# Kernel optimization log

Measured on AMD Instinct MI355X. Metric: run time of the kernel, lower is better.

## Reference

```python
import jax, jax.numpy as jnp
import numpy as np

N_NODES = 100000
IN_DIM = 500
HID_DIM = 128
OUT_DIM = 40
N_EDGES = 1600000


def setup_inputs() -> dict:
    key = jax.random.key(0)
    k1, k2, k3, k4, k5 = jax.random.split(key, 5)
    x = jax.random.normal(k1, (N_NODES, IN_DIM), dtype=jnp.float32)
    edge_index = jax.random.randint(k2, (2, N_EDGES), 0, N_NODES, dtype=jnp.int64)
    # Glorot-style init for linear weights, zero bias (as in PyG GCNConv)
    W1 = jax.random.normal(k3, (IN_DIM, HID_DIM), dtype=jnp.float32) / np.sqrt(IN_DIM)
    b1 = jnp.zeros((HID_DIM,), dtype=jnp.float32)
    W2 = jax.random.normal(k4, (HID_DIM, OUT_DIM), dtype=jnp.float32) / np.sqrt(HID_DIM)
    b2 = jnp.zeros((OUT_DIM,), dtype=jnp.float32)
    return {"x": x, "edge_index": edge_index, "W1": W1, "b1": b1, "W2": W2, "b2": b2}


def reference(x, edge_index, W1, b1, W2, b2):
    N = x.shape[0]
    # GCNConv: add self-loops, symmetric normalization deg^-1/2 A deg^-1/2
    loops = jnp.arange(N, dtype=edge_index.dtype)
    src = jnp.concatenate([edge_index[0], loops])  # [E+N]
    dst = jnp.concatenate([edge_index[1], loops])  # [E+N]
    deg = jax.ops.segment_sum(jnp.ones_like(dst, dtype=x.dtype), dst, num_segments=N)
    dinv = jnp.where(deg > 0, jax.lax.rsqrt(deg), 0.0)
    norm = (dinv[src] * dinv[dst])[:, None]  # [E+N, 1]

    def gcn_conv(h, W, b):
        h = h @ W                              # [N, F_out] linear first (PyG order)
        msg = h[src] * norm                    # gather + scale: [E+N, F_out]
        agg = jax.ops.segment_sum(msg, dst, num_segments=N)  # scatter-add
        return agg + b

    h = jax.nn.relu(gcn_conv(x, W1, b1))
    # dropout(p=0.5) is identity in eval mode
    h = gcn_conv(h, W2, b2)
    return jax.nn.log_softmax(h, axis=1)
```

## Files before the change

kernel.cpp:

```cpp
#include <hip/hip_runtime.h>
#include <hip/hip_bf16.h>

#define IN_DIM 500
#define HID 128
#define OUTD 40
#define KPAD 512

typedef _Float16 f16x8 __attribute__((ext_vector_type(8)));
typedef float f32x16 __attribute__((ext_vector_type(16)));
typedef unsigned short u16x8 __attribute__((ext_vector_type(8)));
typedef unsigned short u16x4 __attribute__((ext_vector_type(4)));

static __device__ __forceinline__ float rsqrt_acc(float x) {
  float r = rsqrtf(x);
  return r * (1.5f - 0.5f * x * r * r);
}

static __device__ __forceinline__ unsigned short h16_of(float f) {
  _Float16 h = (_Float16)f;
  return __builtin_bit_cast(unsigned short, h);
}
static __device__ __forceinline__ float h16_back(unsigned short u) {
  return (float)__builtin_bit_cast(_Float16, u);
}

__global__ void zero_kernel(int* __restrict__ p, int n) {
  int i = blockIdx.x * 256 + threadIdx.x;
  if (i < n) p[i] = 0;
}

__global__ void hist_kernel(const int* __restrict__ dst, int* __restrict__ deg, int E) {
  int e4 = (blockIdx.x * 256 + threadIdx.x) * 4;
  if (e4 + 4 <= E) {
    int4 d = *(const int4*)&dst[e4];
    atomicAdd(&deg[d.x], 1);
    atomicAdd(&deg[d.y], 1);
    atomicAdd(&deg[d.z], 1);
    atomicAdd(&deg[d.w], 1);
  } else {
    for (int e = e4; e < E; e++) atomicAdd(&deg[dst[e]], 1);
  }
}

__global__ void dinv_kernel(const int* __restrict__ deg, float* __restrict__ dinv, int N) {
  int n = blockIdx.x * 256 + threadIdx.x;
  if (n < N) dinv[n] = rsqrt_acc((float)deg[n] + 1.0f);
}

__global__ void scan_a(const int* __restrict__ deg, int* __restrict__ partial,
                       int* __restrict__ blockSums, int N) {
  __shared__ int sums[256];
  int t = threadIdx.x;
  int base = blockIdx.x * 1024 + t * 4;
  int v0 = (base + 0) < N ? deg[base + 0] : 0;
  int v1 = (base + 1) < N ? deg[base + 1] : 0;
  int v2 = (base + 2) < N ? deg[base + 2] : 0;
  int v3 = (base + 3) < N ? deg[base + 3] : 0;
  int l0 = v0, l1 = l0 + v1, l2 = l1 + v2, l3 = l2 + v3;
  sums[t] = l3;
  __syncthreads();
  for (int o = 1; o < 256; o <<= 1) {
    int a = sums[t];
    int b = (t >= o) ? sums[t - o] : 0;
    __syncthreads();
    sums[t] = a + b;
    __syncthreads();
  }
  int excl = sums[t] - l3;
  if (t == 0) blockSums[blockIdx.x] = sums[255];
  if (base + 0 < N) partial[base + 0] = excl;
  if (base + 1 < N) partial[base + 1] = excl + l0;
  if (base + 2 < N) partial[base + 2] = excl + l1;
  if (base + 3 < N) partial[base + 3] = excl + l2;
}

__global__ void scan_b(int* __restrict__ blockSums, int nb) {
  __shared__ int s[256];
  int t = threadIdx.x;
  int orig = (t < nb) ? blockSums[t] : 0;
  s[t] = orig;
  __syncthreads();
  for (int o = 1; o < 256; o <<= 1) {
    int a = s[t];
    int b = (t >= o) ? s[t - o] : 0;
    __syncthreads();
    s[t] = a + b;
    __syncthreads();
  }
  if (t < nb) blockSums[t] = s[t] - orig;
}

__global__ void scan_c(int* __restrict__ row_ptr, const int* __restrict__ blockOff,
                       int* __restrict__ cursor, int N, int E) {
  int n = blockIdx.x * 256 + threadIdx.x;
  if (n < N) {
    int v = row_ptr[n] + blockOff[n >> 10];
    row_ptr[n] = v;
    cursor[n] = v;
  }
  if (n == 0 && blockIdx.x == 0) row_ptr[N] = E;
}

__global__ void place_kernel(const int* __restrict__ src, const int* __restrict__ dst,
                             const float* __restrict__ dinv, int* __restrict__ cursor,
                             int2* __restrict__ ePair, int E) {
  int e2 = (blockIdx.x * 256 + threadIdx.x) * 2;
  if (e2 + 2 <= E) {
    int2 s = *(const int2*)&src[e2];
    int2 d = *(const int2*)&dst[e2];
    int p0 = atomicAdd(&cursor[d.x], 1);
    ePair[p0] = make_int2(s.x, __float_as_int(dinv[s.x] * dinv[d.x]));
    int p1 = atomicAdd(&cursor[d.y], 1);
    ePair[p1] = make_int2(s.y, __float_as_int(dinv[s.y] * dinv[d.y]));
  } else if (e2 < E) {
    int s = src[e2], d = dst[e2];
    int pos = atomicAdd(&cursor[d], 1);
    ePair[pos] = make_int2(s, __float_as_int(dinv[s] * dinv[d]));
  }
}

__global__ void convW1_kernel(const float* __restrict__ W1, unsigned short* __restrict__ Wh) {
  int idx = blockIdx.x * 256 + threadIdx.x;
  if (idx >= HID * KPAD) return;
  int n = idx >> 9, k = idx & (KPAD - 1);
  float f = (k < IN_DIM) ? W1[(size_t)k * HID + n] : 0.f;
  Wh[idx] = h16_of(f);
}

#define LSTR 136

__global__ __launch_bounds__(256) void gemm1_kernel(const float* __restrict__ X,
                                                    const unsigned short* __restrict__ Wh,
                                                    unsigned short* __restrict__ H1, int N) {
  __shared__ unsigned short sA[64 * LSTR];
  __shared__ unsigned short sB[128 * LSTR];
  const int t = threadIdx.x;
  const int rowBase = blockIdx.x * 64;
  const int lane = t & 63;
  const int w = t >> 6;
  const int rw = w & 1;
  const int cw = w >> 1;
  const int m = lane & 31;
  const int quad = lane >> 5;

  f32x16 acc[2];
  acc[0] = (f32x16)(0.f);
  acc[1] = (f32x16)(0.f);

  const int arow8 = t >> 5;
  const int alane = t & 31;
  const int brow16 = t >> 4;
  const int blane = t & 15;

  for (int k0 = 0; k0 < KPAD; k0 += 128) {
    __syncthreads();
    {
      const int kk = k0 + alane * 4;
#pragma unroll
      for (int p = 0; p < 8; p++) {
        const int r = p * 8 + arow8;
        const int grow = rowBase + r;
        float4 v = make_float4(0.f, 0.f, 0.f, 0.f);
        if (grow < N && kk + 4 <= IN_DIM) {
          v = *(const float4*)&X[(size_t)grow * IN_DIM + kk];
        } else if (grow < N && kk < IN_DIM) {
          const float* xr = &X[(size_t)grow * IN_DIM];
          v.x = xr[kk];
          if (kk + 1 < IN_DIM) v.y = xr[kk + 1];
          if (kk + 2 < IN_DIM) v.z = xr[kk + 2];
          if (kk + 3 < IN_DIM) v.w = xr[kk + 3];
        }
        ushort4 hv;
        hv.x = h16_of(v.x); hv.y = h16_of(v.y); hv.z = h16_of(v.z); hv.w = h16_of(v.w);
        *(ushort4*)&sA[r * LSTR + alane * 4] = hv;
      }
    }
    {
#pragma unroll
      for (int p = 0; p < 8; p++) {
        const int r = p * 16 + brow16;
        uint4 bv = *(const uint4*)&Wh[(size_t)r * KPAD + k0 + blane * 8];
        *(uint4*)&sB[r * LSTR + blane * 8] = bv;
      }
    }
    __syncthreads();

#pragma unroll
    for (int sub = 0; sub < 8; sub++) {
      const int ks = sub * 16 + quad * 8;
      f16x8 av = *(const f16x8*)&sA[(rw * 32 + m) * LSTR + ks];
#pragma unroll
      for (int nt = 0; nt < 2; nt++) {
        f16x8 bv = *(const f16x8*)&sB[(cw * 64 + nt * 32 + m) * LSTR + ks];
        acc[nt] = __builtin_amdgcn_mfma_f32_32x32x16_f16(av, bv, acc[nt], 0, 0, 0);
      }
    }
  }

#pragma unroll
  for (int nt = 0; nt < 2; nt++) {
#pragma unroll
    for (int r = 0; r < 16; r++) {
      int rowin = (r & 3) + 8 * (r >> 2) + 4 * quad;
      int grow = rowBase + rw * 32 + rowin;
      if (grow < N) H1[(size_t)grow * HID + cw * 64 + nt * 32 + m] = h16_of(acc[nt][r]);
    }
  }
}

__global__ void agg1_kernel(const unsigned short* __restrict__ h1, const int* __restrict__ row_ptr,
                            const int2* __restrict__ ePair, const float* __restrict__ dinv,
                            const float* __restrict__ b1, unsigned short* __restrict__ hrelu, int N) {
  int gid = blockIdx.x * 256 + threadIdx.x;
  int n = gid >> 4, c8 = (gid & 15) * 8;
  if (n >= N) return;
  float di = dinv[n];
  float sl = di * di;
  float acc[8];
  u16x8 sv = *(const u16x8*)&h1[(size_t)n * HID + c8];
#pragma unroll
  for (int j = 0; j < 8; j++) acc[j] = sl * h16_back(sv[j]);
  int i = row_ptr[n];
  const int s1 = row_ptr[n + 1];
  for (; i + 4 <= s1; i += 4) {
    int2 e0 = ePair[i], e1 = ePair[i + 1], e2 = ePair[i + 2], e3 = ePair[i + 3];
    float w0 = __int_as_float(e0.y), w1 = __int_as_float(e1.y);
    float w2 = __int_as_float(e2.y), w3 = __int_as_float(e3.y);
    u16x8 v0 = *(const u16x8*)&h1[(size_t)e0.x * HID + c8];
    u16x8 v1 = *(const u16x8*)&h1[(size_t)e1.x * HID + c8];
    u16x8 v2 = *(const u16x8*)&h1[(size_t)e2.x * HID + c8];
    u16x8 v3 = *(const u16x8*)&h1[(size_t)e3.x * HID + c8];
#pragma unroll
    for (int j = 0; j < 8; j++) {
      acc[j] += w0 * h16_back(v0[j]) + w1 * h16_back(v1[j]) +
                w2 * h16_back(v2[j]) + w3 * h16_back(v3[j]);
    }
  }
  for (; i < s1; i++) {
    int2 e = ePair[i];
    float w = __int_as_float(e.y);
    u16x8 v = *(const u16x8*)&h1[(size_t)e.x * HID + c8];
#pragma unroll
    for (int j = 0; j < 8; j++) acc[j] += w * h16_back(v[j]);
  }
  u16x8 r;
#pragma unroll
  for (int j = 0; j < 8; j++) {
    float v = fmaxf(acc[j] + b1[c8 + j], 0.f);
    r[j] = h16_of(v);
  }
  *(u16x8*)&hrelu[(size_t)n * HID + c8] = r;
}

__global__ __launch_bounds__(256) void gemm2_kernel(const unsigned short* __restrict__ A,
                                                    const float* __restrict__ W2,
                                                    unsigned short* __restrict__ H2, int N) {
  __shared__ float tA[64 * 129];
  __shared__ float w2s[128 * 48];
  const int t = threadIdx.x;
  const int rowBase = blockIdx.x * 64;
  for (int idx = t; idx < 128 * 48; idx += 256) {
    int k = idx / 48, c = idx - k * 48;
    w2s[idx] = (c < OUTD) ? W2[k * OUTD + c] : 0.f;
  }
  for (int f = t; f < 1024; f += 256) {
    int row = f >> 4, c8 = (f & 15) * 8;
    u16x8 v = (u16x8)(0);
    if (rowBase + row < N) v = *(const u16x8*)&A[(size_t)(rowBase + row) * HID + c8];
#pragma unroll
    for (int j = 0; j < 8; j++) tA[row * 129 + c8 + j] = h16_back(v[j]);
  }
  __syncthreads();
  const int row = t >> 2;
  const int c0 = (t & 3) * 12;
  float acc[12];
#pragma unroll
  for (int j = 0; j < 12; j++) acc[j] = 0.f;
  for (int k = 0; k < HID; k++) {
    float a = tA[row * 129 + k];
    const float* bp = &w2s[k * 48 + c0];
#pragma unroll
    for (int j = 0; j < 12; j++) acc[j] += a * bp[j];
  }
  int r = rowBase + row;
  if (r < N) {
#pragma unroll
    for (int j = 0; j < 12; j++) {
      int c = c0 + j;
      if (c < OUTD) H2[(size_t)r * OUTD + c] = h16_of(acc[j]);
    }
  }
}

__global__ void agg2_kernel(const unsigned short* __restrict__ h2, const int* __restrict__ row_ptr,
                            const int2* __restrict__ ePair, const float* __restrict__ dinv,
                            const float* __restrict__ b2, float* __restrict__ out, int N) {
  int gid = blockIdx.x * 256 + threadIdx.x;
  int n = gid / 10;
  int c4 = (gid - n * 10) * 4;
  if (n >= N) return;
  float di = dinv[n];
  float sl = di * di;
  float acc[4];
  u16x4 sv = *(const u16x4*)&h2[(size_t)n * OUTD + c4];
#pragma unroll
  for (int j = 0; j < 4; j++) acc[j] = sl * h16_back(sv[j]);
  int i = row_ptr[n];
  const int s1 = row_ptr[n + 1];
  for (; i + 4 <= s1; i += 4) {
    int2 e0 = ePair[i], e1 = ePair[i + 1], e2 = ePair[i + 2], e3 = ePair[i + 3];
    float w0 = __int_as_float(e0.y), w1 = __int_as_float(e1.y);
    float w2 = __int_as_float(e2.y), w3 = __int_as_float(e3.y);
    u16x4 v0 = *(const u16x4*)&h2[(size_t)e0.x * OUTD + c4];
    u16x4 v1 = *(const u16x4*)&h2[(size_t)e1.x * OUTD + c4];
    u16x4 v2 = *(const u16x4*)&h2[(size_t)e2.x * OUTD + c4];
    u16x4 v3 = *(const u16x4*)&h2[(size_t)e3.x * OUTD + c4];
#pragma unroll
    for (int j = 0; j < 4; j++) {
      acc[j] += w0 * h16_back(v0[j]) + w1 * h16_back(v1[j]) +
                w2 * h16_back(v2[j]) + w3 * h16_back(v3[j]);
    }
  }
  for (; i < s1; i++) {
    int2 e = ePair[i];
    float w = __int_as_float(e.y);
    u16x4 v = *(const u16x4*)&h2[(size_t)e.x * OUTD + c4];
#pragma unroll
    for (int j = 0; j < 4; j++) acc[j] += w * h16_back(v[j]);
  }
  float* o = &out[(size_t)n * OUTD + c4];
#pragma unroll
  for (int j = 0; j < 4; j++) o[j] = acc[j] + b2[c4 + j];
}

__global__ void lsm_kernel(float* __restrict__ out, int N) {
  int n = blockIdx.x * 256 + threadIdx.x;
  if (n >= N) return;
  float* row = out + (size_t)n * OUTD;
  float v[OUTD];
  float m = -3.4e38f;
#pragma unroll
  for (int j = 0; j < OUTD; j++) {
    v[j] = row[j];
    m = fmaxf(m, v[j]);
  }
  float s = 0.f;
#pragma unroll
  for (int j = 0; j < OUTD; j++) s += expf(v[j] - m);
  float lse = m + logf(s);
#pragma unroll
  for (int j = 0; j < OUTD; j++) row[j] = v[j] - lse;
}

extern "C" void kernel_launch(void* const* d_in, const int* in_sizes, int n_in,
                              void* d_out, int out_size, void* d_ws, size_t ws_size,
                              hipStream_t stream) {
  const float* x  = (const float*)d_in[0];
  const int*   ei = (const int*)d_in[1];
  const float* W1 = (const float*)d_in[2];
  const float* b1 = (const float*)d_in[3];
  const float* W2 = (const float*)d_in[4];
  const float* b2 = (const float*)d_in[5];
  float* out = (float*)d_out;

  const int N = in_sizes[0] / IN_DIM;
  const int E = in_sizes[1] / 2;
  const int* src = ei;
  const int* dst = ei + E;

  char* wsb = (char*)d_ws;
  size_t off = 0;
  auto alloc = [&](size_t bytes) -> char* {
    char* p = wsb + off;
    off = (off + bytes + 1023) & ~(size_t)1023;
    return p;
  };
  int*   deg       = (int*)alloc((size_t)N * 4);
  float* dinv      = (float*)alloc((size_t)N * 4);
  int*   blockSums = (int*)alloc(1024);
  int*   row_ptr   = (int*)alloc((size_t)(N + 1) * 4);
  int*   cursor    = (int*)alloc((size_t)N * 4);
  int2*  ePair     = (int2*)alloc((size_t)E * 8);
  unsigned short* Wh = (unsigned short*)alloc((size_t)HID * KPAD * 2);
  unsigned short* h1h    = (unsigned short*)alloc((size_t)N * HID * 2);
  unsigned short* hreluh = (unsigned short*)alloc((size_t)N * HID * 2);
  unsigned short* h2h    = h1h;
  (void)n_in; (void)out_size;

  if (off > ws_size) return;

  const int gE = (E + 255) / 256;
  const int gN = (N + 255) / 256;
  const int nb = (N + 1023) / 1024;

  zero_kernel<<<gN, 256, 0, stream>>>(deg, N);
  hist_kernel<<<(E / 4 + 255) / 256, 256, 0, stream>>>(dst, deg, E);
  dinv_kernel<<<gN, 256, 0, stream>>>(deg, dinv, N);
  scan_a<<<nb, 256, 0, stream>>>(deg, row_ptr, blockSums, N);
  scan_b<<<1, 256, 0, stream>>>(blockSums, nb);
  scan_c<<<gN, 256, 0, stream>>>(row_ptr, blockSums, cursor, N, E);
  place_kernel<<<(E / 2 + 255) / 256, 256, 0, stream>>>(src, dst, dinv, cursor, ePair, E);
  convW1_kernel<<<(HID * KPAD + 255) / 256, 256, 0, stream>>>(W1, Wh);

  gemm1_kernel<<<(N + 63) / 64, 256, 0, stream>>>(x, Wh, h1h, N);
  agg1_kernel<<<(N * 16 + 255) / 256, 256, 0, stream>>>(h1h, row_ptr, ePair, dinv, b1, hreluh, N);
  gemm2_kernel<<<(N + 63) / 64, 256, 0, stream>>>(hreluh, W2, h2h, N);
  agg2_kernel<<<(N * 10 + 255) / 256, 256, 0, stream>>>(h2h, row_ptr, ePair, dinv, b2, out, N);
  lsm_kernel<<<gN, 256, 0, stream>>>(out, N);
}
```

Baseline: 637.7 us.

## Load GEMM1 operands directly from global memory into MFMA registers, dropping LDS staging

```diff
diff --git a/kernel.cpp b/kernel.cpp
--- a/kernel.cpp
+++ b/kernel.cpp
@@ -127,13 +127,9 @@
   Wh[idx] = h16_of(f);
 }
 
-#define LSTR 136
-
 __global__ __launch_bounds__(256) void gemm1_kernel(const float* __restrict__ X,
                                                     const unsigned short* __restrict__ Wh,
                                                     unsigned short* __restrict__ H1, int N) {
-  __shared__ unsigned short sA[64 * LSTR];
-  __shared__ unsigned short sB[128 * LSTR];
   const int t = threadIdx.x;
   const int rowBase = blockIdx.x * 64;
   const int lane = t & 63;
@@ -147,54 +143,40 @@
   acc[0] = (f32x16)(0.f);
   acc[1] = (f32x16)(0.f);
 
-  const int arow8 = t >> 5;
-  const int alane = t & 31;
-  const int brow16 = t >> 4;
-  const int blane = t & 15;
-
-  for (int k0 = 0; k0 < KPAD; k0 += 128) {
-    __syncthreads();
-    {
-      const int kk = k0 + alane * 4;
-#pragma unroll
-      for (int p = 0; p < 8; p++) {
-        const int r = p * 8 + arow8;
-        const int grow = rowBase + r;
-        float4 v = make_float4(0.f, 0.f, 0.f, 0.f);
-        if (grow < N && kk + 4 <= IN_DIM) {
-          v = *(const float4*)&X[(size_t)grow * IN_DIM + kk];
-        } else if (grow < N && kk < IN_DIM) {
-          const float* xr = &X[(size_t)grow * IN_DIM];
-          v.x = xr[kk];
-          if (kk + 1 < IN_DIM) v.y = xr[kk + 1];
-          if (kk + 2 < IN_DIM) v.z = xr[kk + 2];
-          if (kk + 3 < IN_DIM) v.w = xr[kk + 3];
-        }
-        ushort4 hv;
-        hv.x = h16_of(v.x); hv.y = h16_of(v.y); hv.z = h16_of(v.z); hv.w = h16_of(v.w);
-        *(ushort4*)&sA[r * LSTR + alane * 4] = hv;
-      }
-    }
-    {
-#pragma unroll
-      for (int p = 0; p < 8; p++) {
-        const int r = p * 16 + brow16;
-        uint4 bv = *(const uint4*)&Wh[(size_t)r * KPAD + k0 + blane * 8];
-        *(uint4*)&sB[r * LSTR + blane * 8] = bv;
-      }
-    }
-    __syncthreads();
-
-#pragma unroll
-    for (int sub = 0; sub < 8; sub++) {
-      const int ks = sub * 16 + quad * 8;
-      f16x8 av = *(const f16x8*)&sA[(rw * 32 + m) * LSTR + ks];
-#pragma unroll
-      for (int nt = 0; nt < 2; nt++) {
-        f16x8 bv = *(const f16x8*)&sB[(cw * 64 + nt * 32 + m) * LSTR + ks];
-        acc[nt] = __builtin_amdgcn_mfma_f32_32x32x16_f16(av, bv, acc[nt], 0, 0, 0);
-      }
-    }
+  const int arow = rowBase + rw * 32 + m;
+  const bool aok = arow < N;
+  const float* xr = X + (size_t)(aok ? arow : 0) * IN_DIM;
+  const unsigned short* w0p = Wh + (size_t)(cw * 64 + m) * KPAD;
+  const unsigned short* w1p = Wh + (size_t)(cw * 64 + 32 + m) * KPAD;
+
+#pragma unroll 4
+  for (int ks = 0; ks < 31; ks++) {
+    const int k = ks * 16 + quad * 8;
+    float4 a0 = *(const float4*)&xr[k];
+    float4 a1 = *(const float4*)&xr[k + 4];
+    f16x8 av;
+    av[0] = (_Float16)a0.x; av[1] = (_Float16)a0.y;
+    av[2] = (_Float16)a0.z; av[3] = (_Float16)a0.w;
+    av[4] = (_Float16)a1.x; av[5] = (_Float16)a1.y;
+    av[6] = (_Float16)a1.z; av[7] = (_Float16)a1.w;
+    f16x8 b0 = *(const f16x8*)&w0p[k];
+    f16x8 b1 = *(const f16x8*)&w1p[k];
+    acc[0] = __builtin_amdgcn_mfma_f32_32x32x16_f16(av, b0, acc[0], 0, 0, 0);
+    acc[1] = __builtin_amdgcn_mfma_f32_32x32x16_f16(av, b1, acc[1], 0, 0, 0);
+  }
+  {
+    const int k = 496 + quad * 8;
+    float4 a0 = make_float4(0.f, 0.f, 0.f, 0.f);
+    if (quad == 0) a0 = *(const float4*)&xr[496];
+    f16x8 av;
+    av[0] = (_Float16)a0.x; av[1] = (_Float16)a0.y;
+    av[2] = (_Float16)a0.z; av[3] = (_Float16)a0.w;
+    av[4] = (_Float16)0.f; av[5] = (_Float16)0.f;
+    av[6] = (_Float16)0.f; av[7] = (_Float16)0.f;
+    f16x8 b0 = *(const f16x8*)&w0p[k];
+    f16x8 b1 = *(const f16x8*)&w1p[k];
+    acc[0] = __builtin_amdgcn_mfma_f32_32x32x16_f16(av, b0, acc[0], 0, 0, 0);
+    acc[1] = __builtin_amdgcn_mfma_f32_32x32x16_f16(av, b1, acc[1], 0, 0, 0);
   }
 
 #pragma unroll
```

Result: slower. 697.3 us (+9.3%).
